# Kernel tuning notes

Measured on AMD Instinct MI355X. Metric: run time of the kernel, lower is better.

The kernel has to match this reference:

```python
import jax, jax.numpy as jnp
import numpy as np
from jax import lax

PRE_NMS = 2000
POST_NMS = 300
NMS_THRESH = 0.7
MIN_SIZE = 16.0
SCALE = 1.0
RATIOS = (0.5, 1.0, 2.0)
SCALES = (8, 16, 32)
STRIDES = (8, 16, 32)
FEAT_HW = ((100, 100), (50, 50), (25, 25))
BASE_SIZE = 16.0


def _anchor_base(scale):
    py = px = BASE_SIZE / 2.0
    ab = np.zeros((len(RATIOS), 4), dtype=np.float32)
    for i, r in enumerate(RATIOS):
        h = BASE_SIZE * scale * np.sqrt(r)
        w = BASE_SIZE * scale * np.sqrt(1.0 / r)
        ab[i] = [py - h / 2.0, px - w / 2.0, py + h / 2.0, px + w / 2.0]
    return ab


def _enum_anchors():
    out = []
    for lvl in range(3):
        ab = _anchor_base(SCALES[lvl])
        hh, ww = FEAT_HW[lvl]
        fs = STRIDES[lvl]
        sy = np.arange(0, hh * fs, fs)
        sx = np.arange(0, ww * fs, fs)
        sx, sy = np.meshgrid(sx, sy)
        shift = np.stack((sy.ravel(), sx.ravel(), sy.ravel(), sx.ravel()), axis=1)
        a = ab[None, :, :] + shift[:, None, :]  # [K, A, 4]
        out.append(a.reshape(-1, 4).astype(np.float32))
    return np.concatenate(out, axis=0)  # [39375, 4]


def setup_inputs() -> dict:
    key = jax.random.key(0)
    ks = jax.random.split(key, 8)
    inp = {
        "feat0": jax.random.normal(ks[0], (2, 256, 100, 100), jnp.float32),
        "feat1": jax.random.normal(ks[1], (2, 256, 50, 50), jnp.float32),
        "feat2": jax.random.normal(ks[2], (2, 256, 25, 25), jnp.float32),
        "conv_w": 0.01 * jax.random.normal(ks[3], (256, 256, 3, 3), jnp.float32),
        "conv_b": jnp.zeros((256,), jnp.float32),
        "score_w": 0.01 * jax.random.normal(ks[4], (6, 256), jnp.float32),
        "score_b": jnp.zeros((6,), jnp.float32),
        "loc_w": 0.01 * jax.random.normal(ks[5], (12, 256), jnp.float32),
        "loc_b": jnp.zeros((12,), jnp.float32),
        "anchors": jnp.asarray(_enum_anchors()),
        "img_h": 800,
        "img_w": 800,
    }
    return inp


def loc2bbox(anchors, loc):
    src_h = anchors[:, 2] - anchors[:, 0]
    src_w = anchors[:, 3] - anchors[:, 1]
    ctr_y = anchors[:, 0] + 0.5 * src_h
    ctr_x = anchors[:, 1] + 0.5 * src_w
    dy, dx, dh, dw = loc[:, 0], loc[:, 1], loc[:, 2], loc[:, 3]
    cy = dy * src_h + ctr_y
    cx = dx * src_w + ctr_x
    h = jnp.exp(dh) * src_h
    w = jnp.exp(dw) * src_w
    return jnp.stack([cy - 0.5 * h, cx - 0.5 * w, cy + 0.5 * h, cx + 0.5 * w], axis=1)


def _iou_matrix(boxes):
    area = (boxes[:, 2] - boxes[:, 0]) * (boxes[:, 3] - boxes[:, 1])
    tl = jnp.maximum(boxes[:, None, :2], boxes[None, :, :2])
    br = jnp.minimum(boxes[:, None, 2:], boxes[None, :, 2:])
    wh = jnp.clip(br - tl, 0.0)
    inter = wh[..., 0] * wh[..., 1]
    return inter / (area[:, None] + area[None, :] - inter + 1e-12)


def _nms_keep(boxes, valid):
    # greedy NMS over score-sorted boxes; returns boolean keep mask
    M = _iou_matrix(boxes)  # [PRE_NMS, PRE_NMS]
    idx = jnp.arange(PRE_NMS)

    def body(i, suppressed):
        sup_later = (~suppressed[i]) & (M[i] > NMS_THRESH) & (idx > i)
        return suppressed | sup_later

    suppressed = lax.fori_loop(0, PRE_NMS, body, ~valid)
    return ~suppressed


def _propose(loc, fg, anchors, img_h, img_w):
    roi = loc2bbox(anchors, loc)  # [S, 4]
    roi = jnp.stack([
        jnp.clip(roi[:, 0], 0.0, float(img_h)),
        jnp.clip(roi[:, 1], 0.0, float(img_w)),
        jnp.clip(roi[:, 2], 0.0, float(img_h)),
        jnp.clip(roi[:, 3], 0.0, float(img_w)),
    ], axis=1)
    hs = roi[:, 2] - roi[:, 0]
    ws = roi[:, 3] - roi[:, 1]
    valid = (hs >= MIN_SIZE * SCALE) & (ws >= MIN_SIZE * SCALE)
    sc = jnp.where(valid, fg, -jnp.inf)
    top_sc, top_idx = lax.top_k(sc, PRE_NMS)
    boxes = roi[top_idx]
    keep = _nms_keep(boxes, jnp.isfinite(top_sc))
    # stable move of kept boxes to the front (indices are unique)
    order = jnp.argsort(jnp.where(keep, jnp.arange(PRE_NMS), PRE_NMS))[:POST_NMS]
    rois = boxes[order] * keep[order][:, None].astype(boxes.dtype)  # zero-pad invalid
    return rois  # [POST_NMS, 4]


def reference(feat0, feat1, feat2, conv_w, conv_b, score_w, score_b, loc_w, loc_b, anchors, img_h, img_w):
    feats = [feat0, feat1, feat2]
    n = feat0.shape[0]
    locs, scores, fgs = [], [], []
    dn = ("NCHW", "OIHW", "NCHW")
    for x in feats:
        h = jax.nn.relu(
            lax.conv_general_dilated(x, conv_w, (1, 1), "SAME", dimension_numbers=dn)
            + conv_b[None, :, None, None]
        )
        hh, ww = h.shape[2], h.shape[3]
        loc = jnp.einsum("nchw,oc->nhwo", h, loc_w) + loc_b  # [n,h,w,12]
        sc = jnp.einsum("nchw,oc->nhwo", h, score_w) + score_b  # [n,h,w,6]
        fg = jax.nn.softmax(sc.reshape(n, hh, ww, 3, 2), axis=-1)[..., 1]
        locs.append(loc.reshape(n, -1, 4))
        scores.append(sc.reshape(n, -1, 2))
        fgs.append(fg.reshape(n, -1))
    rpn_locs = jnp.concatenate(locs, axis=1)      # [n, S, 4]
    rpn_scores = jnp.concatenate(scores, axis=1)  # [n, S, 2]
    rpn_fg = jnp.concatenate(fgs, axis=1)         # [n, S]
    rois = jax.vmap(lambda l, f: _propose(l, f, anchors, img_h, img_w))(rpn_locs, rpn_fg)
    rois = rois.reshape(-1, 4)  # [n*POST_NMS, 4]
    roi_indices = jnp.repeat(jnp.arange(n, dtype=jnp.int32), POST_NMS)
    return rpn_locs, rpn_scores, rois, roi_indices, anchors
```

## Files before the change

### kernel.cpp

```cpp
#include <hip/hip_runtime.h>
#include <hip/hip_fp16.h>
#include <cstdint>
#include <cstddef>

typedef unsigned long long u64;
typedef unsigned int u32;
typedef __attribute__((ext_vector_type(8))) _Float16 f16x8;
typedef __attribute__((ext_vector_type(4))) float f32x4;

#define NANCHORS 39375
#define PRE_NMS  2000
#define POST_NMS 300
#define CAND_CAP 4096
#define MPAD 2048
#define UNEG 0x007FFFFFu

__device__ __forceinline__ u32 f2u(float f) {
  u32 u = __float_as_uint(f);
  return (u & 0x80000000u) ? ~u : (u | 0x80000000u);
}

#define GLOAD16(gp, lp) __builtin_amdgcn_global_load_lds( \
    (const __attribute__((address_space(1))) u32*)(const void*)(gp), \
    (__attribute__((address_space(3))) u32*)(void*)(lp), 16, 0, 0)

__global__ __launch_bounds__(256) void xsplit_kernel(
    const float* __restrict__ f0, const float* __restrict__ f1, const float* __restrict__ f2,
    short* __restrict__ xh, short* __restrict__ xl)
{
  __shared__ float tile[64][65];
  int t = blockIdx.x;
  int HW, W, W2, np; const float* fp; int AB, ABS;
  if (t < 1256)      { HW = 10000; W = 100; W2 = 102; np = 157; fp = f0; AB = 0;       ABS = 2663424; }
  else if (t < 1576) { t -= 1256; HW = 2500; W = 50; W2 = 52; np = 40; fp = f1; AB = 5326848; ABS = 692224; }
  else               { t -= 1576; HW = 625;  W = 25; W2 = 27; np = 10; fp = f2; AB = 6711296; ABS = 186624; }
  int posb = t % np, r = t / np;
  int ci0 = (r & 3) * 64, b = r >> 2;
  int pos0 = posb * 64;
  int tid = threadIdx.x, lane = tid & 63, w = tid >> 6;
  int rp = pos0 + lane; if (rp >= HW) rp = HW - 1;
  const float* src = fp + (size_t)(b * 256 + ci0) * HW;
#pragma unroll
  for (int p = 0; p < 16; ++p) {
    int cl = w * 16 + p;
    tile[cl][lane] = src[(size_t)cl * HW + rp];
  }
  __syncthreads();
  int pix = tid >> 2, cq = tid & 3;
  int pos = pos0 + pix;
  if (pos < HW) {
    int y = pos / W, x = pos - y * W;
    size_t ob = (size_t)AB + (size_t)b * ABS + ((size_t)((y + 1) * W2 + (x + 1))) * 256 + ci0 + cq * 16;
    __align__(16) short hs[16], ls[16];
#pragma unroll
    for (int j = 0; j < 16; ++j) {
      float v = tile[cq * 16 + j][pix];
      __half h = __float2half(v);
      __half l = __float2half((v - __half2float(h)) * 2048.0f);
      hs[j] = __half_as_short(h);
      ls[j] = __half_as_short(l);
    }
    *(int4*)(xh + ob) = ((int4*)hs)[0];
    *(int4*)(xh + ob + 8) = ((int4*)hs)[1];
    *(int4*)(xl + ob) = ((int4*)ls)[0];
    *(int4*)(xl + ob + 8) = ((int4*)ls)[1];
  }
}

__global__ __launch_bounds__(256) void wsplit_kernel(
    const float* __restrict__ w, short* __restrict__ wh, short* __restrict__ wl)
{
  int idx = blockIdx.x * 256 + threadIdx.x;
  int tap = idx >> 16, co = (idx >> 8) & 255, ci = idx & 255;
  float v = w[(size_t)co * 2304 + ci * 9 + tap];
  __half h = __float2half(v);
  __half l = __float2half((v - __half2float(h)) * 2048.0f);
  wh[idx] = __half_as_short(h);
  wl[idx] = __half_as_short(l);
}

__global__ __launch_bounds__(256, 2) void gemmconv_kernel(
    const short* __restrict__ xh, const short* __restrict__ xl,
    const short* __restrict__ wh, const short* __restrict__ wl,
    const float* __restrict__ bias, float* __restrict__ hbase)
{
  __shared__ __align__(16) short smem[32768];

  int lb = (blockIdx.x & 7) * 52 + (blockIdx.x >> 3);
  int HW, W, W2, AB, ABS; size_t hoff;
  if (lb < 316)      { HW = 10000; W = 100; W2 = 102; AB = 0;       ABS = 2663424; hoff = 0; }
  else if (lb < 396) { lb -= 316; HW = 2500; W = 50; W2 = 52; AB = 5326848; ABS = 692224; hoff = 5120000; }
  else               { lb -= 396; HW = 625;  W = 25; W2 = 27; AB = 6711296; ABS = 186624; hoff = 6400000; }
  int mb = lb >> 2, b = (lb >> 1) & 1, nb = lb & 1;
  int pos0 = mb * 128, co0 = nb * 128;

  int tid = threadIdx.x;
  int s = tid & 7, mrow = tid >> 3;
  int aoff[4], boff[4];
#pragma unroll
  for (int i = 0; i < 4; ++i) {
    int m = i * 32 + mrow;
    int pos = pos0 + m; if (pos >= HW) pos = HW - 1;
    int y = pos / W, x = pos - y * W;
    aoff[i] = AB + b * ABS + (y * W2 + x) * 256 + ((s ^ (m & 7)) << 3);
    boff[i] = ((co0 + m) << 8) + ((s ^ (m & 7)) << 3);
  }
  int wv = tid >> 6, lane = tid & 63;
  int lr = lane & 15, lk = lane >> 4;
  int wr = wv >> 1, wc = wv & 1;
  int rA0 = wr * 64 + lr, rB0 = wc * 64 + lr;
  int cs = (lr & 7) << 4;
  int c0 = ((lk * 16) ^ cs) >> 1;
  int c1 = ((64 + lk * 16) ^ cs) >> 1;

  f32x4 acc1[4][4], acc2[4][4];
  f32x4 zro = {0.f, 0.f, 0.f, 0.f};
#pragma unroll
  for (int i = 0; i < 4; ++i)
#pragma unroll
    for (int j = 0; j < 4; ++j) { acc1[i][j] = zro; acc2[i][j] = zro; }

  for (int cc = 0; cc < 36; ++cc) {
    int tap = cc >> 2, cq = cc & 3;
    int ty = tap / 3, tx = tap - ty * 3;
    int adel = (ty * W2 + tx) * 256 + (cq << 6);
    int bdel = (tap << 16) + (cq << 6);
    if (cc) __syncthreads();
#pragma unroll
    for (int i = 0; i < 4; ++i) {
      int d = i * 2048 + wv * 512;
      GLOAD16(xh + aoff[i] + adel, smem + d);
      GLOAD16(xl + aoff[i] + adel, smem + 8192 + d);
      GLOAD16(wh + boff[i] + bdel, smem + 16384 + d);
      GLOAD16(wl + boff[i] + bdel, smem + 24576 + d);
    }
    __syncthreads();
#pragma unroll
    for (int k2 = 0; k2 < 2; ++k2) {
      int ck = k2 ? c1 : c0;
      f16x8 ah[4], al[4], bh[4], bl[4];
#pragma unroll
      for (int q = 0; q < 4; ++q) {
        int ro = (rA0 + q * 16) * 64 + ck;
        ah[q] = *(const f16x8*)(smem + ro);
        al[q] = *(const f16x8*)(smem + 8192 + ro);
        int rb = (rB0 + q * 16) * 64 + ck;
        bh[q] = *(const f16x8*)(smem + 16384 + rb);
        bl[q] = *(const f16x8*)(smem + 24576 + rb);
      }
#pragma unroll
      for (int m4 = 0; m4 < 4; ++m4)
#pragma unroll
        for (int n4 = 0; n4 < 4; ++n4) {
          acc1[m4][n4] = __builtin_amdgcn_mfma_f32_16x16x32_f16(ah[m4], bh[n4], acc1[m4][n4], 0, 0, 0);
          acc2[m4][n4] = __builtin_amdgcn_mfma_f32_16x16x32_f16(ah[m4], bl[n4], acc2[m4][n4], 0, 0, 0);
          acc2[m4][n4] = __builtin_amdgcn_mfma_f32_16x16x32_f16(al[m4], bh[n4], acc2[m4][n4], 0, 0, 0);
        }
    }
  }

  float br[4];
#pragma unroll
  for (int n4 = 0; n4 < 4; ++n4) br[n4] = bias[co0 + wc * 64 + n4 * 16 + lr];
  float* outb = hbase + hoff + (size_t)b * HW * 256;
#pragma unroll
  for (int m4 = 0; m4 < 4; ++m4) {
#pragma unroll
    for (int j = 0; j < 4; ++j) {
      int pos = pos0 + wr * 64 + m4 * 16 + lk * 4 + j;
      if (pos < HW) {
        float* op = outb + (size_t)pos * 256 + co0 + wc * 64 + lr;
#pragma unroll
        for (int n4 = 0; n4 < 4; ++n4)
          op[n4 * 16] = acc1[m4][n4][j] + acc2[m4][n4][j] * 4.8828125e-4f + br[n4];
      }
    }
  }
}

__global__ __launch_bounds__(256) void head_kernel(
    const float* __restrict__ hbase, const float* __restrict__ loc_w, const float* __restrict__ loc_b,
    const float* __restrict__ score_w, const float* __restrict__ score_b,
    const float* __restrict__ anchors, const int* __restrict__ imgh, const int* __restrict__ imgw,
    float* __restrict__ out_locs, float* __restrict__ out_scores,
    float* __restrict__ boxes, u32* __restrict__ ukey)
{
  int wid = (blockIdx.x * blockDim.x + threadIdx.x) >> 6;
  int lane = threadIdx.x & 63;
  if (wid >= 2 * 13125) return;
  int b = wid / 13125, r = wid % 13125;
  int HW, pos, base_row; size_t hoff;
  if (r < 10000)      { HW = 10000; pos = r;         base_row = 0;     hoff = 0; }
  else if (r < 12500) { HW = 2500;  pos = r - 10000; base_row = 30000; hoff = 5120000; }
  else                { HW = 625;   pos = r - 12500; base_row = 37500; hoff = 6400000; }

  const float4* hp = (const float4*)(hbase + hoff + ((size_t)b * HW + pos) * 256);
  float4 hv = hp[lane];
  hv.x = fmaxf(hv.x, 0.f); hv.y = fmaxf(hv.y, 0.f);
  hv.z = fmaxf(hv.z, 0.f); hv.w = fmaxf(hv.w, 0.f);

  float s[18];
#pragma unroll
  for (int o = 0; o < 12; ++o) {
    float4 wv = ((const float4*)(loc_w + o * 256))[lane];
    s[o] = hv.x * wv.x + hv.y * wv.y + hv.z * wv.z + hv.w * wv.w;
  }
#pragma unroll
  for (int o = 0; o < 6; ++o) {
    float4 wv = ((const float4*)(score_w + o * 256))[lane];
    s[12 + o] = hv.x * wv.x + hv.y * wv.y + hv.z * wv.z + hv.w * wv.w;
  }
#pragma unroll
  for (int off = 32; off > 0; off >>= 1) {
#pragma unroll
    for (int o = 0; o < 18; ++o) s[o] += __shfl_xor(s[o], off, 64);
  }

  if (lane < 3) {
    int a = lane;
    float l0 = s[4*a+0] + loc_b[4*a+0];
    float l1 = s[4*a+1] + loc_b[4*a+1];
    float l2 = s[4*a+2] + loc_b[4*a+2];
    float l3 = s[4*a+3] + loc_b[4*a+3];
    float sc0 = s[12+2*a+0] + score_b[2*a+0];
    float sc1 = s[12+2*a+1] + score_b[2*a+1];

    int row = base_row + pos * 3 + a;
    size_t g = (size_t)b * NANCHORS + row;
    out_locs[g*4+0] = l0; out_locs[g*4+1] = l1; out_locs[g*4+2] = l2; out_locs[g*4+3] = l3;
    out_scores[g*2+0] = sc0; out_scores[g*2+1] = sc1;

    float mx = fmaxf(sc0, sc1);
    float e0 = expf(sc0 - mx), e1 = expf(sc1 - mx);
    float fg = e1 / (e0 + e1);

    const float* an = anchors + (size_t)row * 4;
    float a0 = an[0], a1 = an[1], a2 = an[2], a3 = an[3];
    float sh = a2 - a0, sw = a3 - a1;
    float cy = a0 + 0.5f * sh, cx = a1 + 0.5f * sw;
    float ncy = l0 * sh + cy, ncx = l1 * sw + cx;
    float nh = expf(l2) * sh, nw = expf(l3) * sw;
    float IH = (float)(*imgh), IW = (float)(*imgw);
    float y1 = fminf(fmaxf(ncy - 0.5f * nh, 0.f), IH);
    float x1 = fminf(fmaxf(ncx - 0.5f * nw, 0.f), IW);
    float y2 = fminf(fmaxf(ncy + 0.5f * nh, 0.f), IH);
    float x2 = fminf(fmaxf(ncx + 0.5f * nw, 0.f), IW);
    bool valid = ((y2 - y1) >= 16.0f) && ((x2 - x1) >= 16.0f);
    float scm = valid ? fg : -__builtin_inff();

    boxes[g*4+0] = y1; boxes[g*4+1] = x1; boxes[g*4+2] = y2; boxes[g*4+3] = x2;
    ukey[g] = f2u(scm);
  }
}

__global__ void copyf_kernel(const float* __restrict__ a, float* __restrict__ o, int n) {
  int t = blockIdx.x * 256 + threadIdx.x;
  if (t < n) o[t] = a[t];
}

__global__ __launch_bounds__(1024) void select_kernel(
    const u32* __restrict__ ukey, u64* __restrict__ cand, int* __restrict__ candcnt)
{
  int b = blockIdx.x, tid = threadIdx.x;
  int wv = tid >> 6;
  const u32* u = ukey + (size_t)b * NANCHORS;
  __shared__ u32 hist[16][256];
  __shared__ u32 scan[256];
  __shared__ u32 sh_prefix;
  __shared__ int sh_rem;
  __shared__ int sh_cnt;

  u32 prefix = 0; int rem = PRE_NMS;
  for (int pass = 0; pass < 4; ++pass) {
    int shift = 24 - 8 * pass;
    for (int i = tid; i < 16 * 256; i += 1024) ((u32*)hist)[i] = 0;
    __syncthreads();
    u32 himask = (pass == 0) ? 0u : (0xFFFFFFFFu << (shift + 8));
    for (int i = tid; i < NANCHORS; i += 1024) {
      u32 v = u[i];
      if ((v & himask) == (prefix & himask))
        atomicAdd(&hist[wv][(v >> shift) & 255u], 1u);
    }
    __syncthreads();
    if (tid < 256) {
      u32 s = 0;
#pragma unroll
      for (int k = 0; k < 16; ++k) s += hist[k][tid];
      scan[tid] = s;
    }
    __syncthreads();
    for (int off = 1; off < 256; off <<= 1) {
      u32 v = 0, add = 0;
      if (tid < 256) { v = scan[tid]; if (tid + off < 256) add = scan[tid + off]; }
      __syncthreads();
      if (tid < 256) scan[tid] = v + add;
      __syncthreads();
    }
    if (tid < 256) {
      int s = (int)scan[tid];
      int snext = (tid < 255) ? (int)scan[tid + 1] : 0;
      if (s >= rem && snext < rem) { sh_prefix = prefix | ((u32)tid << shift); sh_rem = rem - snext; }
    }
    __syncthreads();
    prefix = sh_prefix; rem = sh_rem;
    __syncthreads();
  }

  if (tid == 0) sh_cnt = 0;
  __syncthreads();
  for (int i = tid; i < NANCHORS; i += 1024) {
    u32 v = u[i];
    if (v >= prefix) {
      int p = atomicAdd(&sh_cnt, 1);
      if (p < CAND_CAP)
        cand[(size_t)b * CAND_CAP + p] = ((u64)v << 32) | (u32)(~(u32)i);
    }
  }
  __syncthreads();
  if (tid == 0) candcnt[b] = (sh_cnt < CAND_CAP) ? sh_cnt : CAND_CAP;
}

__global__ __launch_bounds__(1024) void sort_kernel(
    const u64* __restrict__ cand, const int* __restrict__ candcnt,
    const float* __restrict__ boxes, float* __restrict__ topbox, u64* __restrict__ sup0)
{
  int b = blockIdx.x, tid = threadIdx.x;
  __shared__ u64 key[CAND_CAP];
  __shared__ unsigned char validf[2048];
  int cnt = candcnt[b];
  for (int t = tid; t < CAND_CAP; t += 1024)
    key[t] = (t < cnt) ? cand[(size_t)b * CAND_CAP + t] : 0ull;
  __syncthreads();

  u32 n = (cnt <= 2048) ? 2048u : (u32)CAND_CAP;
  for (u32 k = 2; k <= n; k <<= 1) {
    for (u32 j = k >> 1; j > 0; j >>= 1) {
      __syncthreads();
      for (u32 t = tid; t < n; t += 1024) {
        u32 ixj = t ^ j;
        if (ixj > t) {
          u64 a = key[t], c = key[ixj];
          bool desc = ((t & k) == 0);
          if (desc ? (a < c) : (a > c)) { key[t] = c; key[ixj] = a; }
        }
      }
    }
  }
  __syncthreads();

  for (int t = tid; t < 2048; t += 1024) {
    unsigned char vf = 0;
    if (t < PRE_NMS) {
      u64 kk = key[t];
      u32 uu = (u32)(kk >> 32);
      float* tb = topbox + ((size_t)b * PRE_NMS + t) * 4;
      if (uu != 0u) {
        u32 idx = ~((u32)kk);
        const float* bp = boxes + ((size_t)b * NANCHORS + idx) * 4;
        tb[0] = bp[0]; tb[1] = bp[1]; tb[2] = bp[2]; tb[3] = bp[3];
        vf = (uu != UNEG) ? 1 : 0;
      } else {
        tb[0] = 0.f; tb[1] = 0.f; tb[2] = 0.f; tb[3] = 0.f;
      }
    }
    validf[t] = vf;
  }
  __syncthreads();
  if (tid < 32) {
    u64 m = 0;
    for (int bit = 0; bit < 64; ++bit) {
      int j = tid * 64 + bit;
      if (j >= PRE_NMS || !validf[j]) m |= (1ull << bit);
    }
    sup0[b * 32 + tid] = m;
  }
}

__global__ __launch_bounds__(256) void iou_kernel(const float* __restrict__ topbox, u32* __restrict__ M32)
{
  int t = blockIdx.x * 256 + threadIdx.x;
  int b = blockIdx.y;
  int w = t / 2000, i = t % 2000;
  const float* tb = topbox + (size_t)b * PRE_NMS * 4;
  const float* bi = tb + (size_t)i * 4;
  float iy1 = bi[0], ix1 = bi[1], iy2 = bi[2], ix2 = bi[3];
  float ai = (iy2 - iy1) * (ix2 - ix1);
  u64 m = 0;
  for (int bit = 0; bit < 64; ++bit) {
    int j = w * 64 + bit;
    if (j < PRE_NMS && j > i) {
      const float* bj = tb + (size_t)j * 4;
      float ty = fmaxf(iy1, bj[0]), tx = fmaxf(ix1, bj[1]);
      float by = fminf(iy2, bj[2]), bx = fminf(ix2, bj[3]);
      float hh = fmaxf(by - ty, 0.f), ww = fmaxf(bx - tx, 0.f);
      float inter = hh * ww;
      float aj = (bj[2] - bj[0]) * (bj[3] - bj[1]);
      float iou = inter / (ai + aj - inter + 1e-12f);
      if (iou > 0.7f) m |= (1ull << bit);
    }
  }
  u32* out = M32 + (size_t)b * MPAD * 64;
  out[(size_t)(2 * w)     * MPAD + i] = (u32)m;
  out[(size_t)(2 * w + 1) * MPAD + i] = (u32)(m >> 32);
}

__global__ __launch_bounds__(64) void nms_kernel(
    const u32* __restrict__ M32, const u64* __restrict__ sup0, u64* __restrict__ supf)
{
  int b = blockIdx.x;
  int l = threadIdx.x;
  const u32* col = M32 + (size_t)b * MPAD * 64 + (size_t)l * MPAD;
  u32 sup = ((const u32*)sup0)[b * 64 + l];

  uint4 A[16], B[16];
#pragma unroll
  for (int k = 0; k < 16; ++k) A[k] = *(const uint4*)(col + 4 * k);

#define NMS_PROC(buf, cc) do {                                                     \
  _Pragma("unroll")                                                                \
  for (int r = 0; r < 64; ++r) {                                                   \
    u32 d = ((r & 3) == 0) ? buf[r >> 2].x : ((r & 3) == 1) ? buf[r >> 2].y :      \
            ((r & 3) == 2) ? buf[r >> 2].z : buf[r >> 2].w;                        \
    u32 sb = (u32)__builtin_amdgcn_readlane((int)sup, 2 * (cc) + (r >> 5));        \
    u32 m = ((sb >> (r & 31)) & 1u) - 1u;                                          \
    sup |= m & d;                                                                  \
  } } while (0)

  for (int c = 0; c < 32; c += 2) {
#pragma unroll
    for (int k = 0; k < 16; ++k) B[k] = *(const uint4*)(col + (c + 1) * 64 + 4 * k);
    NMS_PROC(A, c);
    if (c + 2 < 32) {
#pragma unroll
      for (int k = 0; k < 16; ++k) A[k] = *(const uint4*)(col + (c + 2) * 64 + 4 * k);
    }
    NMS_PROC(B, c + 1);
  }
  ((u32*)supf)[b * 64 + l] = sup;
}

__global__ __launch_bounds__(320) void final_kernel(
    const u64* __restrict__ supf, const float* __restrict__ topbox,
    float* __restrict__ rois, float* __restrict__ roiidx)
{
  int b = blockIdx.x, tid = threadIdx.x;
  __shared__ int ord[POST_NMS];
  __shared__ int cnt_s;
  if (tid == 0) {
    int cnt = 0;
    for (int w = 0; w < 32 && cnt < POST_NMS; ++w) {
      u64 kept = ~supf[b * 32 + w];
      while (kept && cnt < POST_NMS) {
        int bit = __builtin_ctzll(kept); kept &= kept - 1;
        ord[cnt++] = w * 64 + bit;
      }
    }
    cnt_s = cnt;
  }
  __syncthreads();
  if (tid < POST_NMS) {
    float v0 = 0.f, v1 = 0.f, v2 = 0.f, v3 = 0.f;
    if (tid < cnt_s) {
      const float* tb = topbox + ((size_t)b * PRE_NMS + ord[tid]) * 4;
      v0 = tb[0]; v1 = tb[1]; v2 = tb[2]; v3 = tb[3];
    }
    float* r = rois + ((size_t)b * POST_NMS + tid) * 4;
    r[0] = v0; r[1] = v1; r[2] = v2; r[3] = v3;
    roiidx[b * POST_NMS + tid] = (float)b;
  }
}

extern "C" void kernel_launch(void* const* d_in, const int* in_sizes, int n_in,
                              void* d_out, int out_size, void* d_ws, size_t ws_size,
                              hipStream_t stream) {
  const float* feat0   = (const float*)d_in[0];
  const float* feat1   = (const float*)d_in[1];
  const float* feat2   = (const float*)d_in[2];
  const float* conv_w  = (const float*)d_in[3];
  const float* conv_b  = (const float*)d_in[4];
  const float* score_w = (const float*)d_in[5];
  const float* score_b = (const float*)d_in[6];
  const float* loc_w   = (const float*)d_in[7];
  const float* loc_b   = (const float*)d_in[8];
  const float* anchors = (const float*)d_in[9];
  const int*   img_h   = (const int*)d_in[10];
  const int*   img_w   = (const int*)d_in[11];

  float* out_f       = (float*)d_out;
  float* out_locs    = out_f;
  float* out_scores  = out_f + 315000;
  float* out_rois    = out_f + 472500;
  float* out_roiidx  = out_f + 474900;
  float* out_anchors = out_f + 475500;

  char* p = (char*)d_ws;
  float* hb = (float*)p;      p += (size_t)6720000 * 4;
  short* xth = (short*)p;     p += (size_t)7084544 * 2;
  short* xtl = (short*)p;     p += (size_t)7084544 * 2;
  short* wsh = (short*)p;     p += (size_t)589824 * 2;
  short* wsl = (short*)p;     p += (size_t)589824 * 2;
  float* boxes = (float*)p;   p += (size_t)315000 * 4;
  u32* ukey = (u32*)p;        p += (size_t)78752 * 4;
  u64* cand = (u64*)p;        p += (size_t)2 * CAND_CAP * 8;
  int* candcnt = (int*)p;     p += 256;
  float* topbox = (float*)p;  p += (size_t)16000 * 4;
  u32* M32 = (u32*)p;         p += (size_t)2 * MPAD * 64 * 4;
  u64* sup0 = (u64*)p;        p += 64 * 8;
  u64* supf = (u64*)p;        p += 64 * 8;

  hipMemsetAsync(xth, 0, (size_t)7084544 * 4, stream);
  xsplit_kernel<<<1656, 256, 0, stream>>>(feat0, feat1, feat2, xth, xtl);
  wsplit_kernel<<<2304, 256, 0, stream>>>(conv_w, wsh, wsl);
  gemmconv_kernel<<<416, 256, 0, stream>>>(xth, xtl, wsh, wsl, conv_b, hb);
  head_kernel<<<6563, 256, 0, stream>>>(
      hb, loc_w, loc_b, score_w, score_b, anchors, img_h, img_w,
      out_locs, out_scores, boxes, ukey);
  copyf_kernel<<<(157500 + 255) / 256, 256, 0, stream>>>(anchors, out_anchors, 157500);
  select_kernel<<<2, 1024, 0, stream>>>(ukey, cand, candcnt);
  sort_kernel<<<2, 1024, 0, stream>>>(cand, candcnt, boxes, topbox, sup0);
  iou_kernel<<<dim3(250, 2), 256, 0, stream>>>(topbox, M32);
  nms_kernel<<<2, 64, 0, stream>>>(M32, sup0, supf);
  final_kernel<<<2, 320, 0, stream>>>(supf, topbox, out_rois, out_roiidx);
}
```

Before: 400.6 us.

## Restructure conv GEMM with direct A loads, retile head, fuse select/sort and NMS/final

```diff
diff --git a/kernel.cpp b/kernel.cpp
--- a/kernel.cpp
+++ b/kernel.cpp
@@ -79,12 +79,12 @@
   wl[idx] = __half_as_short(l);
 }
 
-__global__ __launch_bounds__(256, 2) void gemmconv_kernel(
+__global__ __launch_bounds__(512, 2) void gemmconv_kernel(
     const short* __restrict__ xh, const short* __restrict__ xl,
     const short* __restrict__ wh, const short* __restrict__ wl,
     const float* __restrict__ bias, float* __restrict__ hbase)
 {
-  __shared__ __align__(16) short smem[32768];
+  __shared__ __align__(16) short smem[16384];
 
   int lb = (blockIdx.x & 7) * 52 + (blockIdx.x >> 3);
   int HW, W, W2, AB, ABS; size_t hoff;
@@ -95,30 +95,33 @@
   int pos0 = mb * 128, co0 = nb * 128;
 
   int tid = threadIdx.x;
-  int s = tid & 7, mrow = tid >> 3;
-  int aoff[4], boff[4];
-#pragma unroll
-  for (int i = 0; i < 4; ++i) {
-    int m = i * 32 + mrow;
-    int pos = pos0 + m; if (pos >= HW) pos = HW - 1;
-    int y = pos / W, x = pos - y * W;
-    aoff[i] = AB + b * ABS + (y * W2 + x) * 256 + ((s ^ (m & 7)) << 3);
-    boff[i] = ((co0 + m) << 8) + ((s ^ (m & 7)) << 3);
-  }
+  int brow = tid >> 3, s = tid & 7;
+  int boff0 = ((co0 + brow) << 8) + ((s ^ (brow & 7)) << 3);
+  int boff1 = ((co0 + 64 + brow) << 8) + ((s ^ ((64 + brow) & 7)) << 3);
+
   int wv = tid >> 6, lane = tid & 63;
   int lr = lane & 15, lk = lane >> 4;
   int wr = wv >> 1, wc = wv & 1;
-  int rA0 = wr * 64 + lr, rB0 = wc * 64 + lr;
+  int rB0 = wc * 64 + lr;
   int cs = (lr & 7) << 4;
   int c0 = ((lk * 16) ^ cs) >> 1;
   int c1 = ((64 + lk * 16) ^ cs) >> 1;
 
-  f32x4 acc1[4][4], acc2[4][4];
+  int abase[2];
+#pragma unroll
+  for (int q = 0; q < 2; ++q) {
+    int pos = pos0 + wr * 32 + q * 16 + lr;
+    if (pos >= HW) pos = HW - 1;
+    int y = pos / W, x = pos - y * W;
+    abase[q] = AB + b * ABS + (y * W2 + x) * 256 + lk * 8;
+  }
+
+  f32x4 acc1[2][4], acc2[2][4];
   f32x4 zro = {0.f, 0.f, 0.f, 0.f};
 #pragma unroll
-  for (int i = 0; i < 4; ++i)
-#pragma unroll
-    for (int j = 0; j < 4; ++j) { acc1[i][j] = zro; acc2[i][j] = zro; }
+  for (int q = 0; q < 2; ++q)
+#pragma unroll
+    for (int j = 0; j < 4; ++j) { acc1[q][j] = zro; acc2[q][j] = zro; }
 
   for (int cc = 0; cc < 36; ++cc) {
     int tap = cc >> 2, cq = cc & 3;
@@ -126,35 +129,33 @@
     int adel = (ty * W2 + tx) * 256 + (cq << 6);
     int bdel = (tap << 16) + (cq << 6);
     if (cc) __syncthreads();
-#pragma unroll
-    for (int i = 0; i < 4; ++i) {
-      int d = i * 2048 + wv * 512;
-      GLOAD16(xh + aoff[i] + adel, smem + d);
-      GLOAD16(xl + aoff[i] + adel, smem + 8192 + d);
-      GLOAD16(wh + boff[i] + bdel, smem + 16384 + d);
-      GLOAD16(wl + boff[i] + bdel, smem + 24576 + d);
-    }
+    GLOAD16(wh + boff0 + bdel, smem + (wv << 9));
+    GLOAD16(wh + boff1 + bdel, smem + 4096 + (wv << 9));
+    GLOAD16(wl + boff0 + bdel, smem + 8192 + (wv << 9));
+    GLOAD16(wl + boff1 + bdel, smem + 12288 + (wv << 9));
     __syncthreads();
 #pragma unroll
     for (int k2 = 0; k2 < 2; ++k2) {
       int ck = k2 ? c1 : c0;
-      f16x8 ah[4], al[4], bh[4], bl[4];
-#pragma unroll
-      for (int q = 0; q < 4; ++q) {
-        int ro = (rA0 + q * 16) * 64 + ck;
-        ah[q] = *(const f16x8*)(smem + ro);
-        al[q] = *(const f16x8*)(smem + 8192 + ro);
-        int rb = (rB0 + q * 16) * 64 + ck;
-        bh[q] = *(const f16x8*)(smem + 16384 + rb);
-        bl[q] = *(const f16x8*)(smem + 24576 + rb);
-      }
-#pragma unroll
-      for (int m4 = 0; m4 < 4; ++m4)
+      f16x8 ah[2], al[2], bh[4], bl[4];
+#pragma unroll
+      for (int q = 0; q < 2; ++q) {
+        ah[q] = *(const f16x8*)(xh + abase[q] + adel + k2 * 32);
+        al[q] = *(const f16x8*)(xl + abase[q] + adel + k2 * 32);
+      }
+#pragma unroll
+      for (int n4 = 0; n4 < 4; ++n4) {
+        int rb = (rB0 + n4 * 16) * 64 + ck;
+        bh[n4] = *(const f16x8*)(smem + rb);
+        bl[n4] = *(const f16x8*)(smem + 8192 + rb);
+      }
+#pragma unroll
+      for (int q = 0; q < 2; ++q)
 #pragma unroll
         for (int n4 = 0; n4 < 4; ++n4) {
-          acc1[m4][n4] = __builtin_amdgcn_mfma_f32_16x16x32_f16(ah[m4], bh[n4], acc1[m4][n4], 0, 0, 0);
-          acc2[m4][n4] = __builtin_amdgcn_mfma_f32_16x16x32_f16(ah[m4], bl[n4], acc2[m4][n4], 0, 0, 0);
-          acc2[m4][n4] = __builtin_amdgcn_mfma_f32_16x16x32_f16(al[m4], bh[n4], acc2[m4][n4], 0, 0, 0);
+          acc1[q][n4] = __builtin_amdgcn_mfma_f32_16x16x32_f16(ah[q], bh[n4], acc1[q][n4], 0, 0, 0);
+          acc2[q][n4] = __builtin_amdgcn_mfma_f32_16x16x32_f16(ah[q], bl[n4], acc2[q][n4], 0, 0, 0);
+          acc2[q][n4] = __builtin_amdgcn_mfma_f32_16x16x32_f16(al[q], bh[n4], acc2[q][n4], 0, 0, 0);
         }
     }
   }
@@ -164,15 +165,15 @@
   for (int n4 = 0; n4 < 4; ++n4) br[n4] = bias[co0 + wc * 64 + n4 * 16 + lr];
   float* outb = hbase + hoff + (size_t)b * HW * 256;
 #pragma unroll
-  for (int m4 = 0; m4 < 4; ++m4) {
+  for (int q = 0; q < 2; ++q) {
 #pragma unroll
     for (int j = 0; j < 4; ++j) {
-      int pos = pos0 + wr * 64 + m4 * 16 + lk * 4 + j;
+      int pos = pos0 + wr * 32 + q * 16 + lk * 4 + j;
       if (pos < HW) {
         float* op = outb + (size_t)pos * 256 + co0 + wc * 64 + lr;
 #pragma unroll
         for (int n4 = 0; n4 < 4; ++n4)
-          op[n4 * 16] = acc1[m4][n4][j] + acc2[m4][n4][j] * 4.8828125e-4f + br[n4];
+          op[n4 * 16] = acc1[q][n4][j] + acc2[q][n4][j] * 4.8828125e-4f + br[n4];
       }
     }
   }
@@ -185,71 +186,104 @@
     float* __restrict__ out_locs, float* __restrict__ out_scores,
     float* __restrict__ boxes, u32* __restrict__ ukey)
 {
-  int wid = (blockIdx.x * blockDim.x + threadIdx.x) >> 6;
-  int lane = threadIdx.x & 63;
-  if (wid >= 2 * 13125) return;
-  int b = wid / 13125, r = wid % 13125;
-  int HW, pos, base_row; size_t hoff;
-  if (r < 10000)      { HW = 10000; pos = r;         base_row = 0;     hoff = 0; }
-  else if (r < 12500) { HW = 2500;  pos = r - 10000; base_row = 30000; hoff = 5120000; }
-  else                { HW = 625;   pos = r - 12500; base_row = 37500; hoff = 6400000; }
-
-  const float4* hp = (const float4*)(hbase + hoff + ((size_t)b * HW + pos) * 256);
-  float4 hv = hp[lane];
-  hv.x = fmaxf(hv.x, 0.f); hv.y = fmaxf(hv.y, 0.f);
-  hv.z = fmaxf(hv.z, 0.f); hv.w = fmaxf(hv.w, 0.f);
-
-  float s[18];
-#pragma unroll
-  for (int o = 0; o < 12; ++o) {
-    float4 wv = ((const float4*)(loc_w + o * 256))[lane];
-    s[o] = hv.x * wv.x + hv.y * wv.y + hv.z * wv.z + hv.w * wv.w;
-  }
-#pragma unroll
-  for (int o = 0; o < 6; ++o) {
-    float4 wv = ((const float4*)(score_w + o * 256))[lane];
-    s[12 + o] = hv.x * wv.x + hv.y * wv.y + hv.z * wv.z + hv.w * wv.w;
-  }
-#pragma unroll
-  for (int off = 32; off > 0; off >>= 1) {
-#pragma unroll
-    for (int o = 0; o < 18; ++o) s[o] += __shfl_xor(s[o], off, 64);
-  }
-
-  if (lane < 3) {
-    int a = lane;
-    float l0 = s[4*a+0] + loc_b[4*a+0];
-    float l1 = s[4*a+1] + loc_b[4*a+1];
-    float l2 = s[4*a+2] + loc_b[4*a+2];
-    float l3 = s[4*a+3] + loc_b[4*a+3];
-    float sc0 = s[12+2*a+0] + score_b[2*a+0];
-    float sc1 = s[12+2*a+1] + score_b[2*a+1];
-
-    int row = base_row + pos * 3 + a;
-    size_t g = (size_t)b * NANCHORS + row;
-    out_locs[g*4+0] = l0; out_locs[g*4+1] = l1; out_locs[g*4+2] = l2; out_locs[g*4+3] = l3;
-    out_scores[g*2+0] = sc0; out_scores[g*2+1] = sc1;
-
-    float mx = fmaxf(sc0, sc1);
-    float e0 = expf(sc0 - mx), e1 = expf(sc1 - mx);
-    float fg = e1 / (e0 + e1);
-
-    const float* an = anchors + (size_t)row * 4;
-    float a0 = an[0], a1 = an[1], a2 = an[2], a3 = an[3];
-    float sh = a2 - a0, sw = a3 - a1;
-    float cy = a0 + 0.5f * sh, cx = a1 + 0.5f * sw;
-    float ncy = l0 * sh + cy, ncx = l1 * sw + cx;
-    float nh = expf(l2) * sh, nw = expf(l3) * sw;
+  __shared__ float wT[4 * 1288];
+  int tid = threadIdx.x;
+  for (int idx = tid; idx < 4608; idx += 256) {
+    int o = idx >> 8, c = idx & 255;
+    float v = (o < 12) ? loc_w[o * 256 + c] : score_w[(o - 12) * 256 + c];
+    wT[(c >> 6) * 1288 + (c & 63) * 20 + o] = v;
+  }
+  for (int idx = tid; idx < 512; idx += 256) {
+    int c = idx >> 1, o = 18 + (idx & 1);
+    wT[(c >> 6) * 1288 + (c & 63) * 20 + o] = 0.f;
+  }
+  __syncthreads();
+
+  int t = blockIdx.x;
+  int b = t / 207, r = t % 207;
+  int HW, pos0, base_row; size_t hoff;
+  if (r < 157)      { HW = 10000; pos0 = r * 64;         base_row = 0;     hoff = 0; }
+  else if (r < 197) { HW = 2500;  pos0 = (r - 157) * 64; base_row = 30000; hoff = 5120000; }
+  else              { HW = 625;   pos0 = (r - 197) * 64; base_row = 37500; hoff = 6400000; }
+
+  int px = tid >> 2, q = tid & 3;
+  int pos = pos0 + px;
+  int pc = (pos < HW) ? pos : HW - 1;
+  const float* hp = hbase + hoff + ((size_t)b * HW + pc) * 256 + q * 64;
+  const float* wq = wT + q * 1288;
+
+  f32x4 acc[5];
+#pragma unroll
+  for (int o4 = 0; o4 < 5; ++o4) acc[o4] = (f32x4){0.f, 0.f, 0.f, 0.f};
+
+#pragma unroll 4
+  for (int i = 0; i < 16; ++i) {
+    float4 hv = *(const float4*)(hp + i * 4);
+    float hk[4] = {fmaxf(hv.x, 0.f), fmaxf(hv.y, 0.f), fmaxf(hv.z, 0.f), fmaxf(hv.w, 0.f)};
+#pragma unroll
+    for (int k = 0; k < 4; ++k) {
+      const float4* wrow = (const float4*)(wq + (i * 4 + k) * 20);
+#pragma unroll
+      for (int o4 = 0; o4 < 5; ++o4) {
+        float4 wv = wrow[o4];
+        acc[o4][0] = fmaf(hk[k], wv.x, acc[o4][0]);
+        acc[o4][1] = fmaf(hk[k], wv.y, acc[o4][1]);
+        acc[o4][2] = fmaf(hk[k], wv.z, acc[o4][2]);
+        acc[o4][3] = fmaf(hk[k], wv.w, acc[o4][3]);
+      }
+    }
+  }
+#pragma unroll
+  for (int o4 = 0; o4 < 5; ++o4)
+#pragma unroll
+    for (int cpo = 0; cpo < 4; ++cpo) {
+      float v = acc[o4][cpo];
+      v += __shfl_xor(v, 1, 64);
+      v += __shfl_xor(v, 2, 64);
+      acc[o4][cpo] = v;
+    }
+
+  if (q == 0 && pos < HW) {
+    float sarr[18] = {acc[0][0], acc[0][1], acc[0][2], acc[0][3],
+                      acc[1][0], acc[1][1], acc[1][2], acc[1][3],
+                      acc[2][0], acc[2][1], acc[2][2], acc[2][3],
+                      acc[3][0], acc[3][1], acc[3][2], acc[3][3],
+                      acc[4][0], acc[4][1]};
     float IH = (float)(*imgh), IW = (float)(*imgw);
-    float y1 = fminf(fmaxf(ncy - 0.5f * nh, 0.f), IH);
-    float x1 = fminf(fmaxf(ncx - 0.5f * nw, 0.f), IW);
-    float y2 = fminf(fmaxf(ncy + 0.5f * nh, 0.f), IH);
-    float x2 = fminf(fmaxf(ncx + 0.5f * nw, 0.f), IW);
-    bool valid = ((y2 - y1) >= 16.0f) && ((x2 - x1) >= 16.0f);
-    float scm = valid ? fg : -__builtin_inff();
-
-    boxes[g*4+0] = y1; boxes[g*4+1] = x1; boxes[g*4+2] = y2; boxes[g*4+3] = x2;
-    ukey[g] = f2u(scm);
+#pragma unroll
+    for (int a = 0; a < 3; ++a) {
+      float l0 = sarr[4 * a + 0] + loc_b[4 * a + 0];
+      float l1 = sarr[4 * a + 1] + loc_b[4 * a + 1];
+      float l2 = sarr[4 * a + 2] + loc_b[4 * a + 2];
+      float l3 = sarr[4 * a + 3] + loc_b[4 * a + 3];
+      float sc0 = sarr[12 + 2 * a + 0] + score_b[2 * a + 0];
+      float sc1 = sarr[12 + 2 * a + 1] + score_b[2 * a + 1];
+
+      int row = base_row + pos * 3 + a;
+      size_t g = (size_t)b * NANCHORS + row;
+      *(float4*)(out_locs + g * 4) = make_float4(l0, l1, l2, l3);
+      out_scores[g * 2 + 0] = sc0; out_scores[g * 2 + 1] = sc1;
+
+      float mx = fmaxf(sc0, sc1);
+      float e0 = expf(sc0 - mx), e1 = expf(sc1 - mx);
+      float fg = e1 / (e0 + e1);
+
+      const float* an = anchors + (size_t)row * 4;
+      float a0 = an[0], a1 = an[1], a2 = an[2], a3 = an[3];
+      float sh = a2 - a0, sw = a3 - a1;
+      float cy = a0 + 0.5f * sh, cx = a1 + 0.5f * sw;
+      float ncy = l0 * sh + cy, ncx = l1 * sw + cx;
+      float nh = expf(l2) * sh, nw = expf(l3) * sw;
+      float y1 = fminf(fmaxf(ncy - 0.5f * nh, 0.f), IH);
+      float x1 = fminf(fmaxf(ncx - 0.5f * nw, 0.f), IW);
+      float y2 = fminf(fmaxf(ncy + 0.5f * nh, 0.f), IH);
+      float x2 = fminf(fmaxf(ncx + 0.5f * nw, 0.f), IW);
+      bool valid = ((y2 - y1) >= 16.0f) && ((x2 - x1) >= 16.0f);
+      float scm = valid ? fg : -__builtin_inff();
+
+      *(float4*)(boxes + g * 4) = make_float4(y1, x1, y2, x2);
+      ukey[g] = f2u(scm);
+    }
   }
 }
 
@@ -258,8 +292,9 @@
   if (t < n) o[t] = a[t];
 }
 
-__global__ __launch_bounds__(1024) void select_kernel(
-    const u32* __restrict__ ukey, u64* __restrict__ cand, int* __restrict__ candcnt)
+__global__ __launch_bounds__(1024) void selectsort_kernel(
+    const u32* __restrict__ ukey, const float* __restrict__ boxes,
+    float* __restrict__ topbox, u64* __restrict__ sup0)
 {
   int b = blockIdx.x, tid = threadIdx.x;
   int wv = tid >> 6;
@@ -269,6 +304,8 @@
   __shared__ u32 sh_prefix;
   __shared__ int sh_rem;
   __shared__ int sh_cnt;
+  __shared__ u64 key[CAND_CAP];
+  __shared__ unsigned char validf[2048];
 
   u32 prefix = 0; int rem = PRE_NMS;
   for (int pass = 0; pass < 4; ++pass) {
@@ -313,23 +350,13 @@
     if (v >= prefix) {
       int p = atomicAdd(&sh_cnt, 1);
       if (p < CAND_CAP)
-        cand[(size_t)b * CAND_CAP + p] = ((u64)v << 32) | (u32)(~(u32)i);
-    }
-  }
-  __syncthreads();
-  if (tid == 0) candcnt[b] = (sh_cnt < CAND_CAP) ? sh_cnt : CAND_CAP;
-}
-
-__global__ __launch_bounds__(1024) void sort_kernel(
-    const u64* __restrict__ cand, const int* __restrict__ candcnt,
-    const float* __restrict__ boxes, float* __restrict__ topbox, u64* __restrict__ sup0)
-{
-  int b = blockIdx.x, tid = threadIdx.x;
-  __shared__ u64 key[CAND_CAP];
-  __shared__ unsigned char validf[2048];
-  int cnt = candcnt[b];
+        key[p] = ((u64)v << 32) | (u32)(~(u32)i);
+    }
+  }
+  __syncthreads();
+  int cnt = (sh_cnt < CAND_CAP) ? sh_cnt : CAND_CAP;
   for (int t = tid; t < CAND_CAP; t += 1024)
-    key[t] = (t < cnt) ? cand[(size_t)b * CAND_CAP + t] : 0ull;
+    if (t >= cnt) key[t] = 0ull;
   __syncthreads();
 
   u32 n = (cnt <= 2048) ? 2048u : (u32)CAND_CAP;
@@ -404,55 +431,53 @@
   out[(size_t)(2 * w + 1) * MPAD + i] = (u32)(m >> 32);
 }
 
-__global__ __launch_bounds__(64) void nms_kernel(
-    const u32* __restrict__ M32, const u64* __restrict__ sup0, u64* __restrict__ supf)
-{
-  int b = blockIdx.x;
-  int l = threadIdx.x;
-  const u32* col = M32 + (size_t)b * MPAD * 64 + (size_t)l * MPAD;
-  u32 sup = ((const u32*)sup0)[b * 64 + l];
-
-  uint4 A[16], B[16];
-#pragma unroll
-  for (int k = 0; k < 16; ++k) A[k] = *(const uint4*)(col + 4 * k);
+__global__ __launch_bounds__(320) void final_kernel(
+    const u32* __restrict__ M32, const u64* __restrict__ sup0, const float* __restrict__ topbox,
+    float* __restrict__ rois, float* __restrict__ roiidx)
+{
+  int b = blockIdx.x, tid = threadIdx.x;
+  __shared__ u32 supl[64];
+  __shared__ int ord[POST_NMS];
+  __shared__ int cnt_s;
+
+  if (tid < 64) {
+    int l = tid;
+    const u32* col = M32 + (size_t)b * MPAD * 64 + (size_t)l * MPAD;
+    u32 sup = ((const u32*)sup0)[b * 64 + l];
+    uint4 A[16], B[16];
+#pragma unroll
+    for (int k = 0; k < 16; ++k) A[k] = *(const uint4*)(col + 4 * k);
 
 #define NMS_PROC(buf, cc) do {                                                     \
   _Pragma("unroll")                                                                \
-  for (int r = 0; r < 64; ++r) {                                                   \
-    u32 d = ((r & 3) == 0) ? buf[r >> 2].x : ((r & 3) == 1) ? buf[r >> 2].y :      \
-            ((r & 3) == 2) ? buf[r >> 2].z : buf[r >> 2].w;                        \
-    u32 sb = (u32)__builtin_amdgcn_readlane((int)sup, 2 * (cc) + (r >> 5));        \
-    u32 m = ((sb >> (r & 31)) & 1u) - 1u;                                          \
+  for (int rr = 0; rr < 64; ++rr) {                                                \
+    u32 d = ((rr & 3) == 0) ? buf[rr >> 2].x : ((rr & 3) == 1) ? buf[rr >> 2].y :  \
+            ((rr & 3) == 2) ? buf[rr >> 2].z : buf[rr >> 2].w;                     \
+    u32 sb = (u32)__builtin_amdgcn_readlane((int)sup, 2 * (cc) + (rr >> 5));       \
+    u32 m = ((sb >> (rr & 31)) & 1u) - 1u;                                         \
     sup |= m & d;                                                                  \
   } } while (0)
 
-  for (int c = 0; c < 32; c += 2) {
-#pragma unroll
-    for (int k = 0; k < 16; ++k) B[k] = *(const uint4*)(col + (c + 1) * 64 + 4 * k);
-    NMS_PROC(A, c);
-    if (c + 2 < 32) {
-#pragma unroll
-      for (int k = 0; k < 16; ++k) A[k] = *(const uint4*)(col + (c + 2) * 64 + 4 * k);
-    }
-    NMS_PROC(B, c + 1);
-  }
-  ((u32*)supf)[b * 64 + l] = sup;
-}
-
-__global__ __launch_bounds__(320) void final_kernel(
-    const u64* __restrict__ supf, const float* __restrict__ topbox,
-    float* __restrict__ rois, float* __restrict__ roiidx)
-{
-  int b = blockIdx.x, tid = threadIdx.x;
-  __shared__ int ord[POST_NMS];
-  __shared__ int cnt_s;
+    for (int c = 0; c < 32; c += 2) {
+#pragma unroll
+      for (int k = 0; k < 16; ++k) B[k] = *(const uint4*)(col + (c + 1) * 64 + 4 * k);
+      NMS_PROC(A, c);
+      if (c + 2 < 32) {
+#pragma unroll
+        for (int k = 0; k < 16; ++k) A[k] = *(const uint4*)(col + (c + 2) * 64 + 4 * k);
+      }
+      NMS_PROC(B, c + 1);
+    }
+    supl[l] = sup;
+  }
+  __syncthreads();
   if (tid == 0) {
     int cnt = 0;
-    for (int w = 0; w < 32 && cnt < POST_NMS; ++w) {
-      u64 kept = ~supf[b * 32 + w];
+    for (int w = 0; w < 64 && cnt < POST_NMS; ++w) {
+      u32 kept = ~supl[w];
       while (kept && cnt < POST_NMS) {
-        int bit = __builtin_ctzll(kept); kept &= kept - 1;
-        ord[cnt++] = w * 64 + bit;
+        int bit = __builtin_ctz(kept); kept &= kept - 1;
+        ord[cnt++] = w * 32 + bit;
       }
     }
     cnt_s = cnt;
@@ -501,24 +526,19 @@
   short* wsl = (short*)p;     p += (size_t)589824 * 2;
   float* boxes = (float*)p;   p += (size_t)315000 * 4;
   u32* ukey = (u32*)p;        p += (size_t)78752 * 4;
-  u64* cand = (u64*)p;        p += (size_t)2 * CAND_CAP * 8;
-  int* candcnt = (int*)p;     p += 256;
   float* topbox = (float*)p;  p += (size_t)16000 * 4;
   u32* M32 = (u32*)p;         p += (size_t)2 * MPAD * 64 * 4;
   u64* sup0 = (u64*)p;        p += 64 * 8;
-  u64* supf = (u64*)p;        p += 64 * 8;
 
   hipMemsetAsync(xth, 0, (size_t)7084544 * 4, stream);
   xsplit_kernel<<<1656, 256, 0, stream>>>(feat0, feat1, feat2, xth, xtl);
   wsplit_kernel<<<2304, 256, 0, stream>>>(conv_w, wsh, wsl);
-  gemmconv_kernel<<<416, 256, 0, stream>>>(xth, xtl, wsh, wsl, conv_b, hb);
-  head_kernel<<<6563, 256, 0, stream>>>(
+  gemmconv_kernel<<<416, 512, 0, stream>>>(xth, xtl, wsh, wsl, conv_b, hb);
+  head_kernel<<<414, 256, 0, stream>>>(
       hb, loc_w, loc_b, score_w, score_b, anchors, img_h, img_w,
       out_locs, out_scores, boxes, ukey);
   copyf_kernel<<<(157500 + 255) / 256, 256, 0, stream>>>(anchors, out_anchors, 157500);
-  select_kernel<<<2, 1024, 0, stream>>>(ukey, cand, candcnt);
-  sort_kernel<<<2, 1024, 0, stream>>>(cand, candcnt, boxes, topbox, sup0);
+  selectsort_kernel<<<2, 1024, 0, stream>>>(ukey, boxes, topbox, sup0);
   iou_kernel<<<dim3(250, 2), 256, 0, stream>>>(topbox, M32);
-  nms_kernel<<<2, 64, 0, stream>>>(M32, sup0, supf);
-  final_kernel<<<2, 320, 0, stream>>>(supf, topbox, out_rois, out_roiidx);
-}
+  final_kernel<<<2, 320, 0, stream>>>(M32, sup0, topbox, out_rois, out_roiidx);
+}
```

Measured after the change: 485.4 us. 1.21x slower.
